# Kernel tuning notes

Hardware: AMD Instinct MI355X
Metric: run time of the kernel (lower is better)

Reference implementation:

```python
import jax, jax.numpy as jnp
import numpy as np

N = 50000   # nodes
E = 800000  # edges
IN, HID, HEADS, OUT = 128, 32, 4, 64
NEG_SLOPE = 0.2


def _gatv2_layer(x, src, dst, Wl, bl, Wr, br, att, bias, res_W, concat):
    """One PyG-style GATv2Conv layer (eval mode, no dropout).
    x: [N, F_in]; att: [H, C]. Returns [N, H*C] if concat else [N, C]."""
    H, C = att.shape
    xl = (x @ Wl + bl).reshape(N, H, C)   # source transform
    xr = (x @ Wr + br).reshape(N, H, C)   # target transform
    e = jax.nn.leaky_relu(xl[src] + xr[dst], NEG_SLOPE)        # [E, H, C]
    logit = jnp.einsum('ehc,hc->eh', e, att)                   # [E, H]
    # segment softmax over incoming edges per destination node
    m = jax.ops.segment_max(logit, dst, num_segments=N)        # [N, H]
    p = jnp.exp(logit - m[dst])
    denom = jax.ops.segment_sum(p, dst, num_segments=N)
    alpha = p / (denom[dst] + 1e-16)                           # [E, H]
    out = jax.ops.segment_sum(xl[src] * alpha[:, :, None], dst, num_segments=N)  # [N, H, C]
    out = out.reshape(N, H * C) if concat else out.mean(axis=1)
    if res_W is not None:
        out = out + x @ res_W
    return out + bias


def _glorot(key, shape):
    fan_in = shape[0] if len(shape) > 1 else shape[-1]
    return jax.random.normal(key, shape, dtype=jnp.float32) / np.sqrt(fan_in)


def setup_inputs() -> dict:
    key = jax.random.key(0)
    ks = iter(jax.random.split(key, 32))
    x = jax.random.normal(next(ks), (N, IN), dtype=jnp.float32)
    edge_index = jax.random.randint(next(ks), (2, E), 0, N, dtype=jnp.int64)
    d = {"x": x, "edge_index": edge_index}
    HC = HEADS * HID  # 128
    # layer 0: IN -> HEADS*HID, concat, residual
    d["Wl0"] = _glorot(next(ks), (IN, HC)); d["bl0"] = jnp.zeros((HC,), jnp.float32)
    d["Wr0"] = _glorot(next(ks), (IN, HC)); d["br0"] = jnp.zeros((HC,), jnp.float32)
    d["att0"] = _glorot(next(ks), (HEADS, HID)); d["b0"] = jnp.zeros((HC,), jnp.float32)
    d["res0"] = _glorot(next(ks), (IN, HC))
    # layer 1: HC -> HEADS*HID, concat, residual
    d["Wl1"] = _glorot(next(ks), (HC, HC)); d["bl1"] = jnp.zeros((HC,), jnp.float32)
    d["Wr1"] = _glorot(next(ks), (HC, HC)); d["br1"] = jnp.zeros((HC,), jnp.float32)
    d["att1"] = _glorot(next(ks), (HEADS, HID)); d["b1"] = jnp.zeros((HC,), jnp.float32)
    d["res1"] = _glorot(next(ks), (HC, HC))
    # layer 2: HC -> OUT, heads=1, concat=False, no residual
    d["Wl2"] = _glorot(next(ks), (HC, OUT)); d["bl2"] = jnp.zeros((OUT,), jnp.float32)
    d["Wr2"] = _glorot(next(ks), (HC, OUT)); d["br2"] = jnp.zeros((OUT,), jnp.float32)
    d["att2"] = _glorot(next(ks), (1, OUT)); d["b2"] = jnp.zeros((OUT,), jnp.float32)
    return d


def reference(x, edge_index,
              Wl0, bl0, Wr0, br0, att0, b0, res0,
              Wl1, bl1, Wr1, br1, att1, b1, res1,
              Wl2, bl2, Wr2, br2, att2, b2):
    src, dst = edge_index[0], edge_index[1]
    h = _gatv2_layer(x, src, dst, Wl0, bl0, Wr0, br0, att0, b0, res0, True)
    h = jax.nn.elu(h)
    h = _gatv2_layer(h, src, dst, Wl1, bl1, Wr1, br1, att1, b1, res1, True)
    h = jax.nn.elu(h)
    return _gatv2_layer(h, src, dst, Wl2, bl2, Wr2, br2, att2, b2, None, False)
```

## Files before the change

### kernel.cpp

```cpp
#include <hip/hip_runtime.h>
#include <math.h>

#define NN 50000
#define EE 800000
#define NB ((NN + 255) / 256)

typedef short v8s __attribute__((ext_vector_type(8)));
typedef float v4f __attribute__((ext_vector_type(4)));

__device__ __forceinline__ ushort f2bf(float f) {
    uint u = __float_as_uint(f);
    uint r = (u + 0x7fffu + ((u >> 16) & 1u)) >> 16;
    return (ushort)r;
}
__device__ __forceinline__ float bf2f(ushort h) {
    return __uint_as_float(((uint)h) << 16);
}
__device__ __forceinline__ float lrelu(float x) {
    return fmaf(0.4f, fabsf(x), 0.6f * x);
}

template <int CTRL>
__device__ __forceinline__ float dppadd(float x) {
    int y = __builtin_amdgcn_update_dpp(0, __float_as_int(x), CTRL, 0xf, 0xf, true);
    return x + __int_as_float(y);
}
__device__ __forceinline__ float sum8(float x) {
    x = dppadd<0xB1>(x);
    x = dppadd<0x4E>(x);
    x = dppadd<0x141>(x);
    return x;
}
__device__ __forceinline__ float sum16(float x) {
    x = sum8(x);
    x = dppadd<0x140>(x);
    return x;
}
__device__ __forceinline__ float expclamp(float t) {
    return __expf(fminf(fmaxf(t, -60.f), 80.f));
}

__global__ __launch_bounds__(256) void k_hist(const int* __restrict__ dst, int* __restrict__ deg) {
    int e = blockIdx.x * 256 + threadIdx.x;
    if (e < EE) atomicAdd(&deg[dst[e]], 1);
}

__global__ __launch_bounds__(256) void k_scan1(const int* __restrict__ deg, int* __restrict__ bsum) {
    __shared__ int sm[4];
    int t = threadIdx.x;
    int idx = blockIdx.x * 256 + t;
    int x = (idx < NN) ? deg[idx] : 0;
    #pragma unroll
    for (int o = 1; o < 64; o <<= 1) x += __shfl_xor(x, o);
    if ((t & 63) == 0) sm[t >> 6] = x;
    __syncthreads();
    if (t == 0) bsum[blockIdx.x] = sm[0] + sm[1] + sm[2] + sm[3];
}

__global__ __launch_bounds__(256) void k_scan3(const int* __restrict__ deg,
                                               const int* __restrict__ bsum,
                                               int* __restrict__ rowptr,
                                               int* __restrict__ cursor) {
    __shared__ int sb[256];
    __shared__ int sm[256];
    int t = threadIdx.x;
    sb[t] = (t < NB) ? bsum[t] : 0;
    __syncthreads();
    for (int o = 1; o < 256; o <<= 1) {
        int a = (t >= o) ? sb[t - o] : 0;
        __syncthreads();
        sb[t] += a;
        __syncthreads();
    }
    const int boff = (blockIdx.x > 0) ? sb[blockIdx.x - 1] : 0;

    int idx = blockIdx.x * 256 + t;
    int v = (idx < NN) ? deg[idx] : 0;
    sm[t] = v;
    __syncthreads();
    for (int o = 1; o < 256; o <<= 1) {
        int a = (t >= o) ? sm[t - o] : 0;
        __syncthreads();
        sm[t] += a;
        __syncthreads();
    }
    int incl = sm[t] + boff;
    if (idx < NN) { rowptr[idx + 1] = incl; cursor[idx] = incl - v; }
    if (idx == 0) rowptr[0] = 0;
}

__global__ __launch_bounds__(256) void k_scatter(const int* __restrict__ src,
                                                 const int* __restrict__ dst,
                                                 int* __restrict__ cursor,
                                                 int* __restrict__ csrc) {
    int e = blockIdx.x * 256 + threadIdx.x;
    if (e < EE) {
        int d = dst[e];
        int pos = atomicAdd(&cursor[d], 1);
        csrc[pos] = src[e];
    }
}

struct WPack {
    const float* W[8];
    ushort* Th[8];
    ushort* Tl[8];
    int fout[8];
};

__global__ __launch_bounds__(256) void k_conv_w(WPack p) {
    int wi = blockIdx.y;
    int fout = p.fout[wi];
    int total = 128 * fout;
    int i = blockIdx.x * 256 + threadIdx.x;
    if (i >= total) return;
    int k = i / fout;
    int n = i - k * fout;
    float f = p.W[wi][i];
    ushort h = f2bf(f);
    float lo = f - bf2f(h);
    int t = n >> 4, m = n & 15, c = k >> 5, quad = (k >> 3) & 3, j = k & 7;
    int flat = ((((t * 4 + c) * 4 + quad) * 16 + m) << 3) + j;
    p.Th[wi][flat] = h;
    p.Tl[wi][flat] = f2bf(lo);
}

template <int FOUT, bool CVT>
__global__ __launch_bounds__(256) void k_gemm_mfma(
    const float* __restrict__ Xf,
    const ushort* __restrict__ Xh, const ushort* __restrict__ Xl,
    const ushort* __restrict__ T0h, const ushort* __restrict__ T0l, const float* __restrict__ B0,
    const ushort* __restrict__ T1h, const ushort* __restrict__ T1l, const float* __restrict__ B1,
    const ushort* __restrict__ T2h, const ushort* __restrict__ T2l,
    ushort* __restrict__ O0b, float* __restrict__ O1, float* __restrict__ O2)
{
    const int lane = threadIdx.x & 63;
    const int wid  = threadIdx.x >> 6;
    const int m    = lane & 15;
    const int quad = lane >> 4;
    const int row0 = blockIdx.x * 64 + wid * 16;
    const int w    = blockIdx.y;

    const ushort* Th[3] = {T0h, T1h, T2h};
    const ushort* Tl[3] = {T0l, T1l, T2l};
    const float*  Bp[3] = {B0, B1, nullptr};
    const ushort* th = Th[w];
    const ushort* tl = Tl[w];
    const float* bias = Bp[w];
    float* Of = (w == 1) ? O1 : O2;

    v8s ah[4], al[4];
    {
        int arow = row0 + m;
        if (arow > NN - 1) arow = NN - 1;
        #pragma unroll
        for (int c = 0; c < 4; ++c) {
            size_t off = (size_t)arow * 128 + c * 32 + quad * 8;
            if constexpr (CVT) {
                float4 f0 = *(const float4*)(Xf + off);
                float4 f1 = *(const float4*)(Xf + off + 4);
                const float fe[8] = {f0.x, f0.y, f0.z, f0.w, f1.x, f1.y, f1.z, f1.w};
                #pragma unroll
                for (int e = 0; e < 8; ++e) {
                    ushort h = f2bf(fe[e]);
                    float lo = fe[e] - bf2f(h);
                    ah[c][e] = (short)h;
                    al[c][e] = (short)(__float_as_uint(lo) >> 16);
                }
            } else {
                ah[c] = *(const v8s*)(Xh + off);
                al[c] = *(const v8s*)(Xl + off);
            }
        }
    }

    #pragma unroll
    for (int t = 0; t < FOUT / 16; ++t) {
        v4f acc = {0.f, 0.f, 0.f, 0.f};
        #pragma unroll
        for (int c = 0; c < 4; ++c) {
            int boff = t * 2048 + (c * 4 + quad) * 128 + m * 8;
            v8s bh = *(const v8s*)(th + boff);
            v8s bl = *(const v8s*)(tl + boff);
            acc = __builtin_amdgcn_mfma_f32_16x16x32_bf16(al[c], bh, acc, 0, 0, 0);
            acc = __builtin_amdgcn_mfma_f32_16x16x32_bf16(ah[c], bl, acc, 0, 0, 0);
            acc = __builtin_amdgcn_mfma_f32_16x16x32_bf16(ah[c], bh, acc, 0, 0, 0);
        }
        const int col = t * 16 + m;
        float badd = bias ? bias[col] : 0.f;
        if (w == 0) {
            #pragma unroll
            for (int j = 0; j < 4; ++j) {
                int r = row0 + quad * 4 + j;
                if (r < NN) O0b[(size_t)r * FOUT + col] = f2bf(acc[j] + badd);
            }
        } else {
            #pragma unroll
            for (int j = 0; j < 4; ++j) {
                int r = row0 + quad * 4 + j;
                if (r < NN) Of[(size_t)r * FOUT + col] = acc[j] + badd;
            }
        }
    }
}

__global__ __launch_bounds__(256) void k_agg01(const ushort* __restrict__ XLb,
                                               const float4* __restrict__ XR4,
                                               const float4* __restrict__ RES4,
                                               const float* __restrict__ att,
                                               const float* __restrict__ bias,
                                               const int* __restrict__ rowptr,
                                               const int* __restrict__ csrc,
                                               ushort* __restrict__ Hh,
                                               ushort* __restrict__ Hl) {
    const int lane = threadIdx.x & 63;
    const int wid = threadIdx.x >> 6;
    const int n = blockIdx.x * 4 + wid;
    if (n >= NN) return;
    const int beg = rowptr[n];
    const int end = rowptr[n + 1];
    const int half = lane >> 5;
    const uint j = lane & 31;

    const float4 xr = XR4[(uint)n * 32u + j];
    const float4 at = ((const float4*)att)[j];
    float4 s = {0.f, 0.f, 0.f, 0.f};
    float d = 0.f;

    int i = beg;
    for (; i + 4 <= end; i += 4) {
        uint sa = (uint)csrc[i + half];
        uint sb = (uint)csrc[i + 2 + half];
        ushort4 ua = *(const ushort4*)(XLb + sa * 128u + 4u * j);
        ushort4 ub = *(const ushort4*)(XLb + sb * 128u + 4u * j);
        {
            float4 va = {bf2f(ua.x), bf2f(ua.y), bf2f(ua.z), bf2f(ua.w)};
            float t0 = lrelu(va.x + xr.x) * at.x;
            t0 = fmaf(lrelu(va.y + xr.y), at.y, t0);
            t0 = fmaf(lrelu(va.z + xr.z), at.z, t0);
            t0 = fmaf(lrelu(va.w + xr.w), at.w, t0);
            float p = expclamp(sum8(t0));
            d += p;
            s.x = fmaf(p, va.x, s.x); s.y = fmaf(p, va.y, s.y);
            s.z = fmaf(p, va.z, s.z); s.w = fmaf(p, va.w, s.w);
        }
        {
            float4 vb = {bf2f(ub.x), bf2f(ub.y), bf2f(ub.z), bf2f(ub.w)};
            float t0 = lrelu(vb.x + xr.x) * at.x;
            t0 = fmaf(lrelu(vb.y + xr.y), at.y, t0);
            t0 = fmaf(lrelu(vb.z + xr.z), at.z, t0);
            t0 = fmaf(lrelu(vb.w + xr.w), at.w, t0);
            float p = expclamp(sum8(t0));
            d += p;
            s.x = fmaf(p, vb.x, s.x); s.y = fmaf(p, vb.y, s.y);
            s.z = fmaf(p, vb.z, s.z); s.w = fmaf(p, vb.w, s.w);
        }
    }
    for (; i < end; i += 2) {
        int ia = i + half;
        if (ia > end - 1) ia = end - 1;
        uint sa = (uint)csrc[ia];
        ushort4 ua = *(const ushort4*)(XLb + sa * 128u + 4u * j);
        float4 va = {bf2f(ua.x), bf2f(ua.y), bf2f(ua.z), bf2f(ua.w)};
        float t0 = lrelu(va.x + xr.x) * at.x;
        t0 = fmaf(lrelu(va.y + xr.y), at.y, t0);
        t0 = fmaf(lrelu(va.z + xr.z), at.z, t0);
        t0 = fmaf(lrelu(va.w + xr.w), at.w, t0);
        float p = expclamp(sum8(t0));
        if (half && (i + 1 >= end)) p = 0.f;
        d += p;
        s.x = fmaf(p, va.x, s.x); s.y = fmaf(p, va.y, s.y);
        s.z = fmaf(p, va.z, s.z); s.w = fmaf(p, va.w, s.w);
    }

    d   += __shfl_xor(d, 32);
    s.x += __shfl_xor(s.x, 32);
    s.y += __shfl_xor(s.y, 32);
    s.z += __shfl_xor(s.z, 32);
    s.w += __shfl_xor(s.w, 32);

    if (half == 0) {
        float inv = (d > 0.f) ? 1.f / d : 0.f;
        float4 rv = RES4[(uint)n * 32u + j];
        float4 bv = ((const float4*)bias)[j];
        float o0 = fmaf(s.x, inv, rv.x + bv.x);
        float o1 = fmaf(s.y, inv, rv.y + bv.y);
        float o2 = fmaf(s.z, inv, rv.z + bv.z);
        float o3 = fmaf(s.w, inv, rv.w + bv.w);
        o0 = o0 > 0.f ? o0 : __expf(o0) - 1.f;
        o1 = o1 > 0.f ? o1 : __expf(o1) - 1.f;
        o2 = o2 > 0.f ? o2 : __expf(o2) - 1.f;
        o3 = o3 > 0.f ? o3 : __expf(o3) - 1.f;
        ushort4 h, l;
        h.x = f2bf(o0); l.x = f2bf(o0 - bf2f(h.x));
        h.y = f2bf(o1); l.y = f2bf(o1 - bf2f(h.y));
        h.z = f2bf(o2); l.z = f2bf(o2 - bf2f(h.z));
        h.w = f2bf(o3); l.w = f2bf(o3 - bf2f(h.w));
        *(ushort4*)(Hh + (uint)n * 128u + 4u * j) = h;
        *(ushort4*)(Hl + (uint)n * 128u + 4u * j) = l;
    }
}

__global__ __launch_bounds__(256) void k_agg2(const ushort* __restrict__ XLb,
                                              const float4* __restrict__ XR4,
                                              const float* __restrict__ att,
                                              const float* __restrict__ bias,
                                              const int* __restrict__ rowptr,
                                              const int* __restrict__ csrc,
                                              float* __restrict__ OUT) {
    const int lane = threadIdx.x & 63;
    const int wid = threadIdx.x >> 6;
    const int n = blockIdx.x * 4 + wid;
    if (n >= NN) return;
    const int beg = rowptr[n];
    const int end = rowptr[n + 1];
    const int q = lane >> 4;
    const uint jj = lane & 15;

    const float4 xr = XR4[(uint)n * 16u + jj];
    const float4 at = ((const float4*)att)[jj];
    float4 s = {0.f, 0.f, 0.f, 0.f};
    float d = 0.f;
    const int e1 = end - 1;

    for (int i = beg; i < end; i += 8) {
        int i0 = i + q;
        int i1 = i + 4 + q;
        uint s0 = (uint)csrc[min(i0, e1)];
        uint s1 = (uint)csrc[min(i1, e1)];
        ushort4 u0 = *(const ushort4*)(XLb + s0 * 64u + 4u * jj);
        ushort4 u1 = *(const ushort4*)(XLb + s1 * 64u + 4u * jj);
        #pragma unroll
        for (int u = 0; u < 2; ++u) {
            ushort4 uv = (u == 0) ? u0 : u1;
            int ii = (u == 0) ? i0 : i1;
            float4 v = {bf2f(uv.x), bf2f(uv.y), bf2f(uv.z), bf2f(uv.w)};
            float t0 = lrelu(v.x + xr.x) * at.x;
            t0 = fmaf(lrelu(v.y + xr.y), at.y, t0);
            t0 = fmaf(lrelu(v.z + xr.z), at.z, t0);
            t0 = fmaf(lrelu(v.w + xr.w), at.w, t0);
            float p = expclamp(sum16(t0));
            if (ii >= end) p = 0.f;
            d += p;
            s.x = fmaf(p, v.x, s.x); s.y = fmaf(p, v.y, s.y);
            s.z = fmaf(p, v.z, s.z); s.w = fmaf(p, v.w, s.w);
        }
    }

    d   += __shfl_xor(d, 16);   d   += __shfl_xor(d, 32);
    s.x += __shfl_xor(s.x, 16); s.x += __shfl_xor(s.x, 32);
    s.y += __shfl_xor(s.y, 16); s.y += __shfl_xor(s.y, 32);
    s.z += __shfl_xor(s.z, 16); s.z += __shfl_xor(s.z, 32);
    s.w += __shfl_xor(s.w, 16); s.w += __shfl_xor(s.w, 32);

    if (lane < 16) {
        float inv = (d > 0.f) ? 1.f / d : 0.f;
        float4 bv = ((const float4*)bias)[jj];
        float4 o;
        o.x = fmaf(s.x, inv, bv.x);
        o.y = fmaf(s.y, inv, bv.y);
        o.z = fmaf(s.z, inv, bv.z);
        o.w = fmaf(s.w, inv, bv.w);
        *(float4*)(OUT + (uint)n * 64u + 4u * jj) = o;
    }
}

extern "C" void kernel_launch(void* const* d_in, const int* in_sizes, int n_in,
                              void* d_out, int out_size, void* d_ws, size_t ws_size,
                              hipStream_t stream) {
    const float* x    = (const float*)d_in[0];
    const int*   ei   = (const int*)d_in[1];
    const int*   esrc = ei;
    const int*   edst = ei + EE;

    const float* Wl0 = (const float*)d_in[2];
    const float* bl0 = (const float*)d_in[3];
    const float* Wr0 = (const float*)d_in[4];
    const float* br0 = (const float*)d_in[5];
    const float* at0 = (const float*)d_in[6];
    const float* b0  = (const float*)d_in[7];
    const float* rs0 = (const float*)d_in[8];
    const float* Wl1 = (const float*)d_in[9];
    const float* bl1 = (const float*)d_in[10];
    const float* Wr1 = (const float*)d_in[11];
    const float* br1 = (const float*)d_in[12];
    const float* at1 = (const float*)d_in[13];
    const float* b1  = (const float*)d_in[14];
    const float* rs1 = (const float*)d_in[15];
    const float* Wl2 = (const float*)d_in[16];
    const float* bl2 = (const float*)d_in[17];
    const float* Wr2 = (const float*)d_in[18];
    const float* br2 = (const float*)d_in[19];
    const float* at2 = (const float*)d_in[20];
    const float* b2  = (const float*)d_in[21];

    float* out = (float*)d_out;

    ushort* XLb = (ushort*)d_ws;
    float* XR  = (float*)(XLb + (size_t)NN * 128);
    float* RES = XR + (size_t)NN * 128;
    ushort* Xh = (ushort*)(RES + (size_t)NN * 128);
    ushort* Xl_ = Xh + (size_t)NN * 128;
    ushort* Wth = Xl_ + (size_t)NN * 128;
    const int wsz[8] = {16384, 16384, 16384, 16384, 16384, 16384, 8192, 8192};
    ushort* th[8]; ushort* tl[8];
    {
        ushort* p = Wth;
        for (int i = 0; i < 8; ++i) { th[i] = p; p += wsz[i]; }
        for (int i = 0; i < 8; ++i) { tl[i] = p; p += wsz[i]; }
    }
    int* deg    = (int*)(Wth + 2 * (6 * 16384 + 2 * 8192));
    int* rowptr = deg + NN;
    int* cursor = rowptr + (NN + 1);
    int* csrc   = cursor + NN;
    int* bsum   = csrc + EE;

    hipMemsetAsync(deg, 0, NN * sizeof(int), stream);
    k_hist<<<(EE + 255) / 256, 256, 0, stream>>>(edst, deg);
    k_scan1<<<NB, 256, 0, stream>>>(deg, bsum);
    k_scan3<<<NB, 256, 0, stream>>>(deg, bsum, rowptr, cursor);
    k_scatter<<<(EE + 255) / 256, 256, 0, stream>>>(esrc, edst, cursor, csrc);

    WPack wp;
    const float* Ws[8] = {Wl0, Wr0, rs0, Wl1, Wr1, rs1, Wl2, Wr2};
    const int fouts[8] = {128, 128, 128, 128, 128, 128, 64, 64};
    for (int i = 0; i < 8; ++i) { wp.W[i] = Ws[i]; wp.Th[i] = th[i]; wp.Tl[i] = tl[i]; wp.fout[i] = fouts[i]; }
    k_conv_w<<<dim3(64, 8), 256, 0, stream>>>(wp);

    const int gemm_gx = (NN + 63) / 64;
    const int agg_grid = (NN + 3) / 4;

    k_gemm_mfma<128, true><<<dim3(gemm_gx, 3), 256, 0, stream>>>(x, nullptr, nullptr,
        th[0], tl[0], bl0, th[1], tl[1], br0, th[2], tl[2], XLb, XR, RES);
    k_agg01<<<agg_grid, 256, 0, stream>>>(XLb, (const float4*)XR, (const float4*)RES,
        at0, b0, rowptr, csrc, Xh, Xl_);

    k_gemm_mfma<128, false><<<dim3(gemm_gx, 3), 256, 0, stream>>>(nullptr, Xh, Xl_,
        th[3], tl[3], bl1, th[4], tl[4], br1, th[5], tl[5], XLb, XR, RES);
    k_agg01<<<agg_grid, 256, 0, stream>>>(XLb, (const float4*)XR, (const float4*)RES,
        at1, b1, rowptr, csrc, Xh, Xl_);

    k_gemm_mfma<64, false><<<dim3(gemm_gx, 2), 256, 0, stream>>>(nullptr, Xh, Xl_,
        th[6], tl[6], bl2, th[7], tl[7], br2, nullptr, nullptr, XLb, XR, nullptr);
    k_agg2<<<agg_grid, 256, 0, stream>>>(XLb, (const float4*)XR, at2, b2, rowptr, csrc, out);
}
```

Before: 417.6 us.

## Build CSR via two-level bucket sort with shared-memory atomics

```diff
diff --git a/kernel.cpp b/kernel.cpp
--- a/kernel.cpp
+++ b/kernel.cpp
@@ -3,7 +3,8 @@
 
 #define NN 50000
 #define EE 800000
-#define NB ((NN + 255) / 256)
+#define NBK 196
+#define EPB 4096
 
 typedef short v8s __attribute__((ext_vector_type(8)));
 typedef float v4f __attribute__((ext_vector_type(4)));
@@ -40,42 +41,28 @@
     return __expf(fminf(fmaxf(t, -60.f), 80.f));
 }
 
-__global__ __launch_bounds__(256) void k_hist(const int* __restrict__ dst, int* __restrict__ deg) {
-    int e = blockIdx.x * 256 + threadIdx.x;
-    if (e < EE) atomicAdd(&deg[dst[e]], 1);
-}
-
-__global__ __launch_bounds__(256) void k_scan1(const int* __restrict__ deg, int* __restrict__ bsum) {
-    __shared__ int sm[4];
+__global__ __launch_bounds__(256) void k_bktcnt(const int* __restrict__ edst,
+                                                int* __restrict__ bcnt) {
+    __shared__ int h[NBK];
     int t = threadIdx.x;
-    int idx = blockIdx.x * 256 + t;
-    int x = (idx < NN) ? deg[idx] : 0;
+    if (t < NBK) h[t] = 0;
+    __syncthreads();
+    int eb = blockIdx.x * EPB;
     #pragma unroll
-    for (int o = 1; o < 64; o <<= 1) x += __shfl_xor(x, o);
-    if ((t & 63) == 0) sm[t >> 6] = x;
-    __syncthreads();
-    if (t == 0) bsum[blockIdx.x] = sm[0] + sm[1] + sm[2] + sm[3];
-}
-
-__global__ __launch_bounds__(256) void k_scan3(const int* __restrict__ deg,
-                                               const int* __restrict__ bsum,
-                                               int* __restrict__ rowptr,
-                                               int* __restrict__ cursor) {
-    __shared__ int sb[256];
+    for (int k = 0; k < EPB / 256; ++k) {
+        int e = eb + k * 256 + t;
+        if (e < EE) atomicAdd(&h[edst[e] >> 8], 1);
+    }
+    __syncthreads();
+    if (t < NBK && h[t]) atomicAdd(&bcnt[t], h[t]);
+}
+
+__global__ __launch_bounds__(256) void k_bscan(const int* __restrict__ bcnt,
+                                               int* __restrict__ bbase,
+                                               int* __restrict__ bcur) {
     __shared__ int sm[256];
     int t = threadIdx.x;
-    sb[t] = (t < NB) ? bsum[t] : 0;
-    __syncthreads();
-    for (int o = 1; o < 256; o <<= 1) {
-        int a = (t >= o) ? sb[t - o] : 0;
-        __syncthreads();
-        sb[t] += a;
-        __syncthreads();
-    }
-    const int boff = (blockIdx.x > 0) ? sb[blockIdx.x - 1] : 0;
-
-    int idx = blockIdx.x * 256 + t;
-    int v = (idx < NN) ? deg[idx] : 0;
+    int v = (t < NBK) ? bcnt[t] : 0;
     sm[t] = v;
     __syncthreads();
     for (int o = 1; o < 256; o <<= 1) {
@@ -84,20 +71,81 @@
         sm[t] += a;
         __syncthreads();
     }
-    int incl = sm[t] + boff;
-    if (idx < NN) { rowptr[idx + 1] = incl; cursor[idx] = incl - v; }
-    if (idx == 0) rowptr[0] = 0;
-}
-
-__global__ __launch_bounds__(256) void k_scatter(const int* __restrict__ src,
-                                                 const int* __restrict__ dst,
-                                                 int* __restrict__ cursor,
-                                                 int* __restrict__ csrc) {
-    int e = blockIdx.x * 256 + threadIdx.x;
-    if (e < EE) {
-        int d = dst[e];
-        int pos = atomicAdd(&cursor[d], 1);
-        csrc[pos] = src[e];
+    if (t < NBK) { int ex = sm[t] - v; bbase[t] = ex; bcur[t] = ex; }
+}
+
+__global__ __launch_bounds__(256) void k_bktplace(const int* __restrict__ esrc,
+                                                  const int* __restrict__ edst,
+                                                  int* __restrict__ bcur,
+                                                  uint* __restrict__ ebuf) {
+    __shared__ int h[NBK];
+    __shared__ int base[NBK];
+    int t = threadIdx.x;
+    if (t < NBK) h[t] = 0;
+    __syncthreads();
+    int eb = blockIdx.x * EPB;
+    int pk[EPB / 256];
+    #pragma unroll
+    for (int k = 0; k < EPB / 256; ++k) {
+        int e = eb + k * 256 + t;
+        pk[k] = -1;
+        if (e < EE) {
+            int b = edst[e] >> 8;
+            int r = atomicAdd(&h[b], 1);
+            pk[k] = (b << 16) | r;
+        }
+    }
+    __syncthreads();
+    if (t < NBK && h[t]) base[t] = atomicAdd(&bcur[t], h[t]);
+    __syncthreads();
+    #pragma unroll
+    for (int k = 0; k < EPB / 256; ++k) {
+        int e = eb + k * 256 + t;
+        if (e < EE) {
+            int b = pk[k] >> 16;
+            int r = pk[k] & 0xFFFF;
+            uint dl = (uint)(edst[e] & 255);
+            ebuf[base[b] + r] = (dl << 16) | (uint)esrc[e];
+        }
+    }
+}
+
+__global__ __launch_bounds__(256) void k_bktfin(const uint* __restrict__ ebuf,
+                                                const int* __restrict__ bbase,
+                                                const int* __restrict__ bcnt,
+                                                int* __restrict__ rowptr,
+                                                int* __restrict__ csrc) {
+    __shared__ int deg[256];
+    __shared__ int sm[256];
+    __shared__ int cur[256];
+    const int b = blockIdx.x;
+    const int t = threadIdx.x;
+    const int eb = bbase[b];
+    const int ec = bcnt[b];
+    deg[t] = 0;
+    __syncthreads();
+    for (int k = t; k < ec; k += 256)
+        atomicAdd(&deg[ebuf[eb + k] >> 16], 1);
+    __syncthreads();
+    int v = deg[t];
+    sm[t] = v;
+    __syncthreads();
+    for (int o = 1; o < 256; o <<= 1) {
+        int a = (t >= o) ? sm[t - o] : 0;
+        __syncthreads();
+        sm[t] += a;
+        __syncthreads();
+    }
+    int node = b * 256 + t;
+    if (node < NN) rowptr[node + 1] = eb + sm[t];
+    if (node == 0) rowptr[0] = 0;
+    cur[t] = sm[t] - v;
+    __syncthreads();
+    for (int k = t; k < ec; k += 256) {
+        uint u = ebuf[eb + k];
+        int nl = (int)(u >> 16);
+        int r = atomicAdd(&cur[nl], 1);
+        csrc[eb + r] = (int)(u & 0xFFFFu);
     }
 }
 
@@ -409,17 +457,19 @@
         for (int i = 0; i < 8; ++i) { th[i] = p; p += wsz[i]; }
         for (int i = 0; i < 8; ++i) { tl[i] = p; p += wsz[i]; }
     }
-    int* deg    = (int*)(Wth + 2 * (6 * 16384 + 2 * 8192));
-    int* rowptr = deg + NN;
-    int* cursor = rowptr + (NN + 1);
-    int* csrc   = cursor + NN;
-    int* bsum   = csrc + EE;
-
-    hipMemsetAsync(deg, 0, NN * sizeof(int), stream);
-    k_hist<<<(EE + 255) / 256, 256, 0, stream>>>(edst, deg);
-    k_scan1<<<NB, 256, 0, stream>>>(deg, bsum);
-    k_scan3<<<NB, 256, 0, stream>>>(deg, bsum, rowptr, cursor);
-    k_scatter<<<(EE + 255) / 256, 256, 0, stream>>>(esrc, edst, cursor, csrc);
+    int* bcnt   = (int*)(Wth + 2 * (6 * 16384 + 2 * 8192));
+    int* bbase  = bcnt + 256;
+    int* bcur   = bbase + 256;
+    int* rowptr = bcur + 256;
+    int* csrc   = rowptr + (NN + 1);
+    uint* ebuf  = (uint*)(csrc + EE);
+
+    hipMemsetAsync(bcnt, 0, 256 * sizeof(int), stream);
+    const int ebk = (EE + EPB - 1) / EPB;
+    k_bktcnt<<<ebk, 256, 0, stream>>>(edst, bcnt);
+    k_bscan<<<1, 256, 0, stream>>>(bcnt, bbase, bcur);
+    k_bktplace<<<ebk, 256, 0, stream>>>(esrc, edst, bcur, ebuf);
+    k_bktfin<<<NBK, 256, 0, stream>>>(ebuf, bbase, bcnt, rowptr, csrc);
 
     WPack wp;
     const float* Ws[8] = {Wl0, Wr0, rs0, Wl1, Wr1, rs1, Wl2, Wr2};
```

Result: faster. 366.5 us (-12.2%).
